# Optimization experiments

Hardware: AMD Instinct MI355X
Metric: run time of the kernel (lower is better)

The kernel has to match this reference:

```python
import jax, jax.numpy as jnp
import numpy as np

N, E, G = 50000, 1600000, 64
F_NODE, F_EDGE, ACT = 128, 16, 10
NEG_SLOPE = 0.2  # GATv2Conv default negative_slope
LAYER_DIMS = [(F_NODE, 32), (32, 64), (64, 128)]


def _glorot(k, shape):
    fan_in, fan_out = shape[0], shape[-1]
    s = jnp.sqrt(6.0 / (fan_in + fan_out))
    return jax.random.uniform(k, shape, jnp.float32, -s, s)


def setup_inputs() -> dict:
    key = jax.random.key(0)
    ks = iter(jax.random.split(key, 64))
    inp = {
        "x": jax.random.normal(next(ks), (N, F_NODE), jnp.float32),
        "edge_attr": jax.random.normal(next(ks), (E, F_EDGE), jnp.float32),
        "edge_index": jax.random.randint(next(ks), (2, E), 0, N, jnp.int32),
        "batch": jnp.sort(jax.random.randint(next(ks), (N,), 0, G, jnp.int32)),
    }
    for i, (din, dout) in enumerate(LAYER_DIMS, 1):
        inp[f"Wl{i}"] = _glorot(next(ks), (din, dout))   # lin_l (source transform)
        inp[f"bl{i}"] = jnp.zeros((dout,), jnp.float32)
        inp[f"Wr{i}"] = _glorot(next(ks), (din, dout))   # lin_r (dest transform)
        inp[f"br{i}"] = jnp.zeros((dout,), jnp.float32)
        inp[f"We{i}"] = _glorot(next(ks), (F_EDGE, dout))  # lin_edge (no bias)
        inp[f"att{i}"] = _glorot(next(ks), (1, dout))[0]   # attention vector
        inp[f"bo{i}"] = jnp.zeros((dout,), jnp.float32)    # output bias
    inp["Wv1"] = _glorot(next(ks), (128, 64)); inp["bv1"] = jnp.zeros((64,), jnp.float32)
    inp["Wv2"] = _glorot(next(ks), (64, 1));   inp["bv2"] = jnp.zeros((1,), jnp.float32)
    inp["Wa1"] = _glorot(next(ks), (128, 64)); inp["ba1"] = jnp.zeros((64,), jnp.float32)
    inp["Wa2"] = _glorot(next(ks), (64, ACT)); inp["ba2"] = jnp.zeros((ACT,), jnp.float32)
    return inp


def _gatv2(x, src, dst, ea, Wl, bl, Wr, br, We, att, bo):
    """GATv2Conv, heads=1, concat=True, edge_dim=F_EDGE (eval mode)."""
    xl = x @ Wl + bl                               # [N, D] source-side
    xr = x @ Wr + br                               # [N, D] dest-side
    m = xl[src] + xr[dst] + ea @ We                # [E, D]
    score = (jax.nn.leaky_relu(m, NEG_SLOPE) * att).sum(-1)  # [E]
    # segment softmax over edges grouped by destination node
    mx = jax.lax.stop_gradient(jax.ops.segment_max(score, dst, num_segments=N))
    ex = jnp.exp(score - mx[dst])
    den = jax.ops.segment_sum(ex, dst, num_segments=N)
    alpha = ex / (den[dst] + 1e-16)                # [E]
    out = jax.ops.segment_sum(alpha[:, None] * xl[src], dst, num_segments=N)
    return out + bo


def _forward(x, edge_attr, src, dst, batch, p):
    h = x
    for i in (1, 2, 3):
        h = jax.nn.relu(_gatv2(h, src, dst, edge_attr,
                               p[f"Wl{i}"], p[f"bl{i}"], p[f"Wr{i}"], p[f"br{i}"],
                               p[f"We{i}"], p[f"att{i}"], p[f"bo{i}"]))
    # global mean pool per graph
    cnt = jax.ops.segment_sum(jnp.ones((N,), h.dtype), batch, num_segments=G)
    pooled = jax.ops.segment_sum(h, batch, num_segments=G) / jnp.maximum(cnt, 1.0)[:, None]
    # dueling heads
    v = jax.nn.relu(pooled @ p["Wv1"] + p["bv1"]) @ p["Wv2"] + p["bv2"]      # [G, 1]
    a = jax.nn.relu(pooled @ p["Wa1"] + p["ba1"]) @ p["Wa2"] + p["ba2"]      # [G, ACT]
    return v + (a - a.mean(axis=1, keepdims=True))


def reference(x, edge_attr, edge_index, batch,
              Wl1, bl1, Wr1, br1, We1, att1, bo1,
              Wl2, bl2, Wr2, br2, We2, att2, bo2,
              Wl3, bl3, Wr3, br3, We3, att3, bo3,
              Wv1, bv1, Wv2, bv2, Wa1, ba1, Wa2, ba2):
    p = dict(Wl1=Wl1, bl1=bl1, Wr1=Wr1, br1=br1, We1=We1, att1=att1, bo1=bo1,
             Wl2=Wl2, bl2=bl2, Wr2=Wr2, br2=br2, We2=We2, att2=att2, bo2=bo2,
             Wl3=Wl3, bl3=bl3, Wr3=Wr3, br3=br3, We3=We3, att3=att3, bo3=bo3,
             Wv1=Wv1, bv1=bv1, Wv2=Wv2, bv2=bv2, Wa1=Wa1, ba1=ba1, Wa2=Wa2, ba2=ba2)
    return _forward(x, edge_attr, edge_index[0], edge_index[1], batch, p)
```

## Files before the change

kernel.cpp:

```cpp
#include <hip/hip_runtime.h>
#include <cstdint>
#include <cstddef>

static constexpr int NN = 50000;
static constexpr int NE = 1600000;
static constexpr int NG = 64;
static constexpr int FE = 16;

typedef float f32x4 __attribute__((ext_vector_type(4)));

template<int DIN, int DOUT>
__global__ __launch_bounds__(256) void k_node_linear(
    const float* __restrict__ h,
    const float* __restrict__ Wl, const float* __restrict__ bl,
    const float* __restrict__ Wr, const float* __restrict__ br,
    float* __restrict__ xl, float* __restrict__ xr)
{
    __shared__ float sW[2 * DIN * DOUT];
    __shared__ float sX[16 * DIN];
    const int n0 = blockIdx.x * 16;

    for (int i = threadIdx.x; i < DIN * DOUT; i += 256) {
        sW[i] = Wl[i];
        sW[DIN * DOUT + i] = Wr[i];
    }
    for (int i = threadIdx.x; i < 16 * DIN; i += 256) {
        int r = i / DIN, k = i % DIN;
        int n = n0 + r;
        sX[i] = (n < NN) ? h[(size_t)n * DIN + k] : 0.0f;
    }
    __syncthreads();

    for (int o = threadIdx.x; o < 16 * DOUT; o += 256) {
        int r = o / DOUT, d = o % DOUT;
        int n = n0 + r;
        if (n >= NN) continue;
        float accl = bl[d], accr = br[d];
        #pragma unroll 8
        for (int k = 0; k < DIN; ++k) {
            float xv = sX[r * DIN + k];
            accl = fmaf(xv, sW[k * DOUT + d], accl);
            accr = fmaf(xv, sW[DIN * DOUT + k * DOUT + d], accr);
        }
        xl[(size_t)n * DOUT + d] = accl;
        xr[(size_t)n * DOUT + d] = accr;
    }
}

__global__ __launch_bounds__(256) void k_count(
    const int* __restrict__ ei, int* __restrict__ cnt)
{
    const int e = blockIdx.x * 256 + threadIdx.x;
    if (e >= NE) return;
    atomicAdd(cnt + ei[NE + e], 1);
}

__global__ __launch_bounds__(1024) void k_scan(
    const int* __restrict__ cnt, int* __restrict__ rowptr)
{
    __shared__ int part[1024];
    const int T = 1024;
    const int C = (NN + T - 1) / T;
    const int t = threadIdx.x;
    const int base = t * C;
    int s = 0;
    for (int i = 0; i < C; ++i) {
        int idx = base + i;
        if (idx < NN) s += cnt[idx];
    }
    part[t] = s;
    __syncthreads();
    for (int off = 1; off < T; off <<= 1) {
        int v = 0;
        if (t >= off) v = part[t - off];
        __syncthreads();
        if (t >= off) part[t] += v;
        __syncthreads();
    }
    int run = (t == 0) ? 0 : part[t - 1];
    for (int i = 0; i < C; ++i) {
        int idx = base + i;
        if (idx < NN) { rowptr[idx] = run; run += cnt[idx]; }
    }
    if (t == T - 1) rowptr[NN] = run;
}

__global__ __launch_bounds__(256) void k_fill(
    const int* __restrict__ ei, const int* __restrict__ rowptr,
    int* __restrict__ woff, int* __restrict__ eids, int* __restrict__ esrc,
    const float* __restrict__ ea, float* __restrict__ eaperm, const int do_perm)
{
    const int e = blockIdx.x * 256 + threadIdx.x;
    if (e >= NE) return;
    const int dst = ei[NE + e];
    const int pos = rowptr[dst] + atomicAdd(woff + dst, 1);
    esrc[pos] = ei[e];
    if (do_perm) {
        const f32x4* s4 = (const f32x4*)(ea + (size_t)e * FE);
        f32x4* d4 = (f32x4*)(eaperm + (size_t)pos * FE);
        d4[0] = s4[0]; d4[1] = s4[1]; d4[2] = s4[2]; d4[3] = s4[3];
    } else {
        eids[pos] = e;
    }
}

template<int D, bool PERM>
__global__ __launch_bounds__(128, 4) void k_gat_fused(
    const int* __restrict__ rowptr, const int* __restrict__ eidx,
    const int* __restrict__ esrc, const float* __restrict__ eaf,
    const float* __restrict__ xl, const float* __restrict__ xr,
    const float* __restrict__ We, const float* __restrict__ att,
    const float* __restrict__ bo, float* __restrict__ hout)
{
    constexpr int SW  = D / 2;
    constexpr int EPW = 64 / SW;
    constexpr int WPB = 2;

    const int wave = threadIdx.x >> 6;
    const int lane = threadIdx.x & 63;
    const int n = blockIdx.x * WPB + wave;
    if (n >= NN) return;
    const int sub = lane / SW;
    const int dl  = lane % SW;
    const int d0  = 2 * dl;

    float rWe[2 * FE], rAtt[2], rXr[2], acc[2];
    {
        const float2 a2 = *(const float2*)(att + d0);
        rAtt[0] = a2.x; rAtt[1] = a2.y;
        const float2 x2 = *(const float2*)(xr + (size_t)n * D + d0);
        rXr[0] = x2.x; rXr[1] = x2.y;
        #pragma unroll
        for (int k = 0; k < FE; ++k) {
            const float2 w2 = *(const float2*)(We + k * D + d0);
            rWe[2 * k] = w2.x; rWe[2 * k + 1] = w2.y;
        }
        acc[0] = acc[1] = 0.f;
    }

    const int p0 = rowptr[n], p1 = rowptr[n + 1];
    float m = -3.4e38f, l = 0.f;

    auto load_edge = [&](int p, float (&eav)[FE], float (&rXl)[2]) {
        const int s = esrc[p];
        const float2 x2 = *(const float2*)(xl + (size_t)s * D + d0);
        rXl[0] = x2.x; rXl[1] = x2.y;
        int erow; if constexpr (PERM) erow = p; else erow = eidx[p];
        if constexpr (SW == 64) {
            const float* ep = eaf + (size_t)(unsigned)__builtin_amdgcn_readfirstlane(erow) * FE;
            #pragma unroll
            for (int k = 0; k < FE; ++k) eav[k] = ep[k];
        } else {
            const float* ep = eaf + (size_t)erow * FE;
            #pragma unroll
            for (int k4 = 0; k4 < 4; ++k4) {
                const float4 v = *(const float4*)(ep + 4 * k4);
                eav[4 * k4]     = v.x; eav[4 * k4 + 1] = v.y;
                eav[4 * k4 + 2] = v.z; eav[4 * k4 + 3] = v.w;
            }
        }
    };
    auto score_edge = [&](const float (&eav)[FE], const float (&rXl)[2]) -> float {
        float m0 = rXl[0] + rXr[0], m1 = rXl[1] + rXr[1];
        #pragma unroll
        for (int k = 0; k < FE; ++k) {
            m0 = fmaf(eav[k], rWe[2 * k], m0);
            m1 = fmaf(eav[k], rWe[2 * k + 1], m1);
        }
        m0 = fmaxf(m0, 0.2f * m0);
        m1 = fmaxf(m1, 0.2f * m1);
        float sv = fmaf(m0, rAtt[0], m1 * rAtt[1]);
        #pragma unroll
        for (int off = 1; off < SW; off <<= 1) sv += __shfl_xor(sv, off);
        return sv;
    };
    auto sm_update = [&](float sv, const float (&rXl)[2]) {
        const float dd = sv - m;
        float wexp;
        if (__builtin_expect(dd > 8.f, 0)) {
            const float r = __expf(-dd);
            acc[0] *= r; acc[1] *= r;
            l *= r; m = sv; wexp = 1.f;
        } else {
            wexp = __expf(dd);
        }
        acc[0] = fmaf(wexp, rXl[0], acc[0]);
        acc[1] = fmaf(wexp, rXl[1], acc[1]);
        l += wexp;
    };

    int p = p0 + sub;
    for (; p + EPW < p1; p += 2 * EPW) {
        float eavA[FE], rXlA[2], eavB[FE], rXlB[2];
        load_edge(p, eavA, rXlA);
        load_edge(p + EPW, eavB, rXlB);
        const float svA = score_edge(eavA, rXlA);
        const float svB = score_edge(eavB, rXlB);
        sm_update(svA, rXlA);
        sm_update(svB, rXlB);
    }
    if (p < p1) {
        float eav[FE], rXl[2];
        load_edge(p, eav, rXl);
        sm_update(score_edge(eav, rXl), rXl);
    }

    #pragma unroll
    for (int step = SW; step < 64; step <<= 1) {
        const float mo = __shfl_xor(m, step);
        const float mstar = fmaxf(m, mo);
        const float sc = __expf(m - mstar);
        acc[0] *= sc; acc[1] *= sc; l *= sc;
        acc[0] += __shfl_xor(acc[0], step);
        acc[1] += __shfl_xor(acc[1], step);
        l += __shfl_xor(l, step);
        m = mstar;
    }

    if (lane < SW) {
        const float inv = 1.0f / (l + 1e-16f);
        const float2 b2 = *(const float2*)(bo + d0);
        float2 o;
        o.x = fmaxf(fmaf(acc[0], inv, b2.x), 0.f);
        o.y = fmaxf(fmaf(acc[1], inv, b2.y), 0.f);
        *(float2*)(hout + (size_t)n * D + d0) = o;
    }
}

__global__ __launch_bounds__(128) void k_pool(
    const float* __restrict__ h, const int* __restrict__ batch,
    float* __restrict__ pooled, float* __restrict__ cnt)
{
    constexpr int BLOCKS = 512;
    constexpr int CH = (NN + BLOCKS - 1) / BLOCKS;
    const int t = threadIdx.x;
    const int n0 = blockIdx.x * CH;
    const int n1 = min(NN, n0 + CH);
    if (n0 >= n1) return;

    int g = batch[n0];
    float acc = 0.f, c = 0.f;
    for (int n = n0; n < n1; ++n) {
        const int bg = batch[n];
        if (bg != g) {
            atomicAdd(pooled + g * 128 + t, acc);
            if (t == 0) atomicAdd(cnt + g, c);
            acc = 0.f; c = 0.f; g = bg;
        }
        acc += h[(size_t)n * 128 + t];
        c += 1.f;
    }
    atomicAdd(pooled + g * 128 + t, acc);
    if (t == 0) atomicAdd(cnt + g, c);
}

__global__ __launch_bounds__(128) void k_head(
    const float* __restrict__ pooled, const float* __restrict__ cnt,
    const float* __restrict__ Wv1, const float* __restrict__ bv1,
    const float* __restrict__ Wv2, const float* __restrict__ bv2,
    const float* __restrict__ Wa1, const float* __restrict__ ba1,
    const float* __restrict__ Wa2, const float* __restrict__ ba2,
    float* __restrict__ out)
{
    __shared__ float pr[128];
    __shared__ float hv[64];
    __shared__ float ha[64];
    __shared__ float sA[10];
    __shared__ float sVM[2];
    const int g = blockIdx.x;
    const int t = threadIdx.x;

    const float inv = 1.0f / fmaxf(cnt[g], 1.0f);
    pr[t] = pooled[g * 128 + t] * inv;
    __syncthreads();

    if (t < 64) {
        float sv = bv1[t], sa = ba1[t];
        #pragma unroll 8
        for (int k = 0; k < 128; ++k) {
            float p = pr[k];
            sv = fmaf(p, Wv1[k * 64 + t], sv);
            sa = fmaf(p, Wa1[k * 64 + t], sa);
        }
        hv[t] = fmaxf(sv, 0.0f);
        ha[t] = fmaxf(sa, 0.0f);
    }
    __syncthreads();

    if (t < 10) {
        float av = ba2[t];
        #pragma unroll
        for (int j = 0; j < 64; ++j) av = fmaf(ha[j], Wa2[j * 10 + t], av);
        sA[t] = av;
    }
    if (t == 64) {
        float v = bv2[0];
        #pragma unroll
        for (int j = 0; j < 64; ++j) v = fmaf(hv[j], Wv2[j], v);
        sVM[0] = v;
    }
    __syncthreads();

    if (t == 0) {
        float s = 0.0f;
        #pragma unroll
        for (int j = 0; j < 10; ++j) s += sA[j];
        sVM[1] = s * 0.1f;
    }
    __syncthreads();

    if (t < 10) out[g * 10 + t] = sVM[0] + sA[t] - sVM[1];
}

extern "C" void kernel_launch(void* const* d_in, const int* in_sizes, int n_in,
                              void* d_out, int out_size, void* d_ws, size_t ws_size,
                              hipStream_t stream)
{
    const float* x     = (const float*)d_in[0];
    const float* ea    = (const float*)d_in[1];
    const int*   ei    = (const int*)d_in[2];
    const int*   batch = (const int*)d_in[3];

    float* ws = (float*)d_ws;
    float* xl     = ws;
    float* xr     = xl + (size_t)NN * 128;
    float* hA     = xr + (size_t)NN * 128;
    float* hB     = hA + (size_t)NN * 128;
    float* pooled = hB + (size_t)NN * 64;
    float* cntp   = pooled + (size_t)NG * 128;
    int*   rowptr = (int*)(cntp + NG);
    int*   cnt    = rowptr + (NN + 1);
    int*   woff   = cnt + NN;
    int*   eids   = woff + NN;
    int*   esrc   = eids + NE;
    float* eaperm = (float*)(esrc + NE);

    const size_t need = ((char*)(eaperm + (size_t)NE * FE)) - (char*)d_ws;
    const bool use_perm = (ws_size >= need);

    const int EB = (NE + 255) / 256;

    hipMemsetAsync(cnt, 0, 2 * NN * sizeof(int), stream);
    k_count<<<dim3(EB), dim3(256), 0, stream>>>(ei, cnt);
    k_scan<<<dim3(1), dim3(1024), 0, stream>>>(cnt, rowptr);
    k_fill<<<dim3(EB), dim3(256), 0, stream>>>(
        ei, rowptr, woff, eids, esrc, ea, eaperm, use_perm ? 1 : 0);

    const int GB = (NN + 1) / 2;

#define LAYER(DIN, DOUT, HIN, HOUT, B)                                                   \
    do {                                                                                 \
        k_node_linear<DIN, DOUT><<<dim3((NN + 15) / 16), dim3(256), 0, stream>>>(        \
            HIN, (const float*)d_in[B], (const float*)d_in[(B) + 1],                     \
            (const float*)d_in[(B) + 2], (const float*)d_in[(B) + 3], xl, xr);           \
        if (use_perm)                                                                    \
            k_gat_fused<DOUT, true><<<dim3(GB), dim3(128), 0, stream>>>(                 \
                rowptr, eids, esrc, eaperm, xl, xr, (const float*)d_in[(B) + 4],         \
                (const float*)d_in[(B) + 5], (const float*)d_in[(B) + 6], HOUT);         \
        else                                                                             \
            k_gat_fused<DOUT, false><<<dim3(GB), dim3(128), 0, stream>>>(                \
                rowptr, eids, esrc, ea, xl, xr, (const float*)d_in[(B) + 4],             \
                (const float*)d_in[(B) + 5], (const float*)d_in[(B) + 6], HOUT);         \
    } while (0)

    LAYER(128, 32, x,  hA, 4);
    LAYER(32,  64, hA, hB, 11);
    LAYER(64, 128, hB, hA, 18);

#undef LAYER

    hipMemsetAsync(pooled, 0, (NG * 128 + NG) * sizeof(float), stream);
    k_pool<<<dim3(512), dim3(128), 0, stream>>>(hA, batch, pooled, cntp);
    k_head<<<dim3(NG), dim3(128), 0, stream>>>(
        pooled, cntp,
        (const float*)d_in[25], (const float*)d_in[26],
        (const float*)d_in[27], (const float*)d_in[28],
        (const float*)d_in[29], (const float*)d_in[30],
        (const float*)d_in[31], (const float*)d_in[32],
        (float*)d_out);
}
```

Measured before the change: 1.003 ms.

## Drop edge-attribute permutation, vectorize node linear, scalarize indices for wide layers

Removes the copy of edge attributes into destination-sorted order and always gathers them through the edge-id indirection, which saves a large 100 MB read+write pass but makes edge-attribute reads in all three layers random instead of sequential. The node linear kernel now computes four output columns per thread with vector LDS loads and stores. For the D=128 layer, row pointers and per-edge indices are forced into scalar registers with readfirstlane. The net effect depends on whether the saved permutation traffic outweighs three layers of scattered 64-byte edge reads.

```diff
diff --git a/kernel.cpp b/kernel.cpp
--- a/kernel.cpp
+++ b/kernel.cpp
@@ -31,19 +31,21 @@
     }
     __syncthreads();
 
-    for (int o = threadIdx.x; o < 16 * DOUT; o += 256) {
-        int r = o / DOUT, d = o % DOUT;
-        int n = n0 + r;
+    constexpr int NQ = DOUT / 4;
+    for (int o = threadIdx.x; o < 16 * NQ; o += 256) {
+        const int r = o / NQ, d0 = 4 * (o % NQ);
+        const int n = n0 + r;
         if (n >= NN) continue;
-        float accl = bl[d], accr = br[d];
-        #pragma unroll 8
+        f32x4 accl = *(const f32x4*)(bl + d0);
+        f32x4 accr = *(const f32x4*)(br + d0);
+        #pragma unroll 4
         for (int k = 0; k < DIN; ++k) {
-            float xv = sX[r * DIN + k];
-            accl = fmaf(xv, sW[k * DOUT + d], accl);
-            accr = fmaf(xv, sW[DIN * DOUT + k * DOUT + d], accr);
-        }
-        xl[(size_t)n * DOUT + d] = accl;
-        xr[(size_t)n * DOUT + d] = accr;
+            const float xv = sX[r * DIN + k];
+            accl += xv * *(const f32x4*)(sW + k * DOUT + d0);
+            accr += xv * *(const f32x4*)(sW + DIN * DOUT + k * DOUT + d0);
+        }
+        *(f32x4*)(xl + (size_t)n * DOUT + d0) = accl;
+        *(f32x4*)(xr + (size_t)n * DOUT + d0) = accr;
     }
 }
 
@@ -87,24 +89,17 @@
 
 __global__ __launch_bounds__(256) void k_fill(
     const int* __restrict__ ei, const int* __restrict__ rowptr,
-    int* __restrict__ woff, int* __restrict__ eids, int* __restrict__ esrc,
-    const float* __restrict__ ea, float* __restrict__ eaperm, const int do_perm)
+    int* __restrict__ woff, int* __restrict__ eids, int* __restrict__ esrc)
 {
     const int e = blockIdx.x * 256 + threadIdx.x;
     if (e >= NE) return;
     const int dst = ei[NE + e];
     const int pos = rowptr[dst] + atomicAdd(woff + dst, 1);
+    eids[pos] = e;
     esrc[pos] = ei[e];
-    if (do_perm) {
-        const f32x4* s4 = (const f32x4*)(ea + (size_t)e * FE);
-        f32x4* d4 = (f32x4*)(eaperm + (size_t)pos * FE);
-        d4[0] = s4[0]; d4[1] = s4[1]; d4[2] = s4[2]; d4[3] = s4[3];
-    } else {
-        eids[pos] = e;
-    }
-}
-
-template<int D, bool PERM>
+}
+
+template<int D>
 __global__ __launch_bounds__(128, 4) void k_gat_fused(
     const int* __restrict__ rowptr, const int* __restrict__ eidx,
     const int* __restrict__ esrc, const float* __restrict__ eaf,
@@ -138,19 +133,27 @@
         acc[0] = acc[1] = 0.f;
     }
 
-    const int p0 = rowptr[n], p1 = rowptr[n + 1];
+    int p0 = rowptr[n], p1 = rowptr[n + 1];
+    if constexpr (SW == 64) {
+        p0 = __builtin_amdgcn_readfirstlane(p0);
+        p1 = __builtin_amdgcn_readfirstlane(p1);
+    }
     float m = -3.4e38f, l = 0.f;
 
     auto load_edge = [&](int p, float (&eav)[FE], float (&rXl)[2]) {
-        const int s = esrc[p];
-        const float2 x2 = *(const float2*)(xl + (size_t)s * D + d0);
-        rXl[0] = x2.x; rXl[1] = x2.y;
-        int erow; if constexpr (PERM) erow = p; else erow = eidx[p];
         if constexpr (SW == 64) {
-            const float* ep = eaf + (size_t)(unsigned)__builtin_amdgcn_readfirstlane(erow) * FE;
+            const int s    = __builtin_amdgcn_readfirstlane(esrc[p]);
+            const int erow = __builtin_amdgcn_readfirstlane(eidx[p]);
+            const float2 x2 = *(const float2*)(xl + (size_t)s * D + d0);
+            rXl[0] = x2.x; rXl[1] = x2.y;
+            const float* ep = eaf + (size_t)(unsigned)erow * FE;
             #pragma unroll
             for (int k = 0; k < FE; ++k) eav[k] = ep[k];
         } else {
+            const int s    = esrc[p];
+            const int erow = eidx[p];
+            const float2 x2 = *(const float2*)(xl + (size_t)s * D + d0);
+            rXl[0] = x2.x; rXl[1] = x2.y;
             const float* ep = eaf + (size_t)erow * FE;
             #pragma unroll
             for (int k4 = 0; k4 < 4; ++k4) {
@@ -333,18 +336,13 @@
     int*   woff   = cnt + NN;
     int*   eids   = woff + NN;
     int*   esrc   = eids + NE;
-    float* eaperm = (float*)(esrc + NE);
-
-    const size_t need = ((char*)(eaperm + (size_t)NE * FE)) - (char*)d_ws;
-    const bool use_perm = (ws_size >= need);
 
     const int EB = (NE + 255) / 256;
 
     hipMemsetAsync(cnt, 0, 2 * NN * sizeof(int), stream);
     k_count<<<dim3(EB), dim3(256), 0, stream>>>(ei, cnt);
     k_scan<<<dim3(1), dim3(1024), 0, stream>>>(cnt, rowptr);
-    k_fill<<<dim3(EB), dim3(256), 0, stream>>>(
-        ei, rowptr, woff, eids, esrc, ea, eaperm, use_perm ? 1 : 0);
+    k_fill<<<dim3(EB), dim3(256), 0, stream>>>(ei, rowptr, woff, eids, esrc);
 
     const int GB = (NN + 1) / 2;
 
@@ -353,14 +351,9 @@
         k_node_linear<DIN, DOUT><<<dim3((NN + 15) / 16), dim3(256), 0, stream>>>(        \
             HIN, (const float*)d_in[B], (const float*)d_in[(B) + 1],                     \
             (const float*)d_in[(B) + 2], (const float*)d_in[(B) + 3], xl, xr);           \
-        if (use_perm)                                                                    \
-            k_gat_fused<DOUT, true><<<dim3(GB), dim3(128), 0, stream>>>(                 \
-                rowptr, eids, esrc, eaperm, xl, xr, (const float*)d_in[(B) + 4],         \
-                (const float*)d_in[(B) + 5], (const float*)d_in[(B) + 6], HOUT);         \
-        else                                                                             \
-            k_gat_fused<DOUT, false><<<dim3(GB), dim3(128), 0, stream>>>(                \
-                rowptr, eids, esrc, ea, xl, xr, (const float*)d_in[(B) + 4],             \
-                (const float*)d_in[(B) + 5], (const float*)d_in[(B) + 6], HOUT);         \
+        k_gat_fused<DOUT><<<dim3(GB), dim3(128), 0, stream>>>(                           \
+            rowptr, eids, esrc, ea, xl, xr, (const float*)d_in[(B) + 4],                 \
+            (const float*)d_in[(B) + 5], (const float*)d_in[(B) + 6], HOUT);             \
     } while (0)
 
     LAYER(128, 32, x,  hA, 4);
```

Result: faster. 888.5 us (-11.4%).
